# Kernel tuning notes

Measured on AMD Instinct MI355X. Metric: run time of the kernel, lower is better.

The kernel has to match this reference:

```python
import jax, jax.numpy as jnp
import numpy as np

DIM = 1024
K = 7
DILATION = 2
BATCH = 16384
NEG_SLOPE = 0.01


def setup_inputs() -> dict:
    key = jax.random.key(0)
    k1, k2, k3, k4 = jax.random.split(key, 4)
    x = jax.random.normal(k1, (BATCH, DIM), dtype=jnp.float32)
    # Conv1d(1,1,K) default init ~ U(-1/sqrt(K), 1/sqrt(K)); normal is fine for a baseline
    weight = jax.random.normal(k2, (1, 1, K), dtype=jnp.float32) * 0.3
    bias = jax.random.normal(k3, (1,), dtype=jnp.float32) * 0.1
    lmbd = jax.random.normal(k4, (DIM,), dtype=jnp.float32)
    return {"x": x, "weight": weight, "bias": bias, "lmbd": lmbd}


def _forward(x, weight, bias, lmbd):
    pad = (K - 1) * DILATION
    padded = jnp.pad(x, ((0, 0), (0, pad)))  # right-pad last dim
    # (B,1,L) conv with dilated kernel (1,1,K), VALID -> output length = DIM
    conv = jax.lax.conv_general_dilated(
        padded[:, None, :], weight,
        window_strides=(1,), padding="VALID", rhs_dilation=(DILATION,),
        dimension_numbers=("NCH", "OIH", "NCH"))
    conv = conv[:, 0, :] + bias[0]  # (B, DIM)

    w = weight.reshape(-1)  # (K,)
    w0 = w[0]

    activation = jnp.where(conv >= 0, conv, NEG_SLOPE * conv)  # leaky_relu
    act_grad = jnp.where(activation >= 0, 1.0, NEG_SLOPE)

    sp = jax.nn.softplus(lmbd)
    scale = jnp.where(w0 == 0, lmbd,
                      jnp.where(w0 > 0, -1.0 / w0 + sp, -1.0 / w0 - sp))  # (DIM,)

    # diag-matmul == broadcasted per-feature scale
    output = activation * scale + x  # skip connection
    act_grad_scaled = act_grad * scale
    logdet = jnp.log(jnp.abs(act_grad_scaled * w0 + 1.0)).sum(axis=1)  # (B,)
    return output, logdet


def reference(x, weight, bias, lmbd):
    return _forward(x, weight, bias, lmbd)
```

## Files before the change

### kernel.cpp

```cpp
#include <hip/hip_runtime.h>
#include <math.h>

#define DIM 1024
#define KK 7
#define DIL 2
#define BATCH 16384
#define NEG 0.01f
#define ROWS 8
#define RST 1040
#define NBUF 3

__device__ __forceinline__ void gload_lds16(const float* g, float* l) {
    __builtin_amdgcn_global_load_lds(
        (const __attribute__((address_space(1))) void*)g,
        (__attribute__((address_space(3))) void*)l, 16, 0, 0);
}

__global__ __launch_bounds__(256)
void cnn_flow_fused(const float* __restrict__ x,
                    const float* __restrict__ wgt,
                    const float* __restrict__ bias,
                    const float* __restrict__ lmbd,
                    float* __restrict__ out,
                    float* __restrict__ logdet) {
    const int t    = threadIdx.x;
    const int wv   = t >> 6;
    const int lane = t & 63;
    const int base = t << 2;
    const int row0 = blockIdx.x * ROWS;

    __shared__ float sx[NBUF * 2 * RST];
    __shared__ float red[ROWS][4];

    const float* gseg = x + (size_t)row0 * DIM + (wv << 8) + (lane << 2);
    float*       lseg = sx + (wv << 8) + (lane << 2);

    if (t < NBUF * 2 * 16)
        sx[(t >> 4) * RST + DIM + (t & 15)] = 0.0f;

    gload_lds16(gseg + 0 * DIM, lseg + 0 * RST);
    gload_lds16(gseg + 1 * DIM, lseg + 1 * RST);

    float w[KK];
#pragma unroll
    for (int k = 0; k < KK; ++k) w[k] = wgt[k];
    const float w0 = w[0];
    const float bs = bias[0];

    float sc[4], lp[4], ln[4];
    {
        float4 lm = *reinterpret_cast<const float4*>(lmbd + base);
        float lms[4] = {lm.x, lm.y, lm.z, lm.w};
        const float inv = (w0 != 0.0f) ? (-1.0f / w0) : 0.0f;
#pragma unroll
        for (int i = 0; i < 4; ++i) {
            float l  = lms[i];
            float sp = fmaxf(l, 0.0f) + log1pf(expf(-fabsf(l)));
            float scale;
            if (w0 == 0.0f)      scale = l;
            else if (w0 > 0.0f)  scale = inv + sp;
            else                 scale = inv - sp;
            sc[i] = scale;
            lp[i] = logf(fabsf(fmaf(scale,       w0, 1.0f)));
            ln[i] = logf(fabsf(fmaf(NEG * scale, w0, 1.0f)));
        }
    }

#pragma unroll
    for (int k = 0; k < ROWS / 2; ++k) {
        if (k < ROWS / 2 - 1) {
            float* lb = sx + ((k + 1) % NBUF) * 2 * RST + (wv << 8) + (lane << 2);
            gload_lds16(gseg + (2 * k + 2) * DIM, lb);
            gload_lds16(gseg + (2 * k + 3) * DIM, lb + RST);
        }
        if (k == 0)
            asm volatile("s_waitcnt vmcnt(2) lgkmcnt(0)" ::: "memory");
        else if (k < ROWS / 2 - 1)
            asm volatile("s_waitcnt vmcnt(4)" ::: "memory");
        else
            asm volatile("s_waitcnt vmcnt(2)" ::: "memory");
        __builtin_amdgcn_s_barrier();

        const float* buf = sx + (k % NBUF) * 2 * RST;
#pragma unroll
        for (int rr = 0; rr < 2; ++rr) {
            const int r = 2 * k + rr;
            const float* srow = buf + rr * RST + base;
            float xv[16];
#pragma unroll
            for (int j = 0; j < 4; ++j) {
                float4 v = *reinterpret_cast<const float4*>(srow + 4 * j);
                xv[4 * j + 0] = v.x; xv[4 * j + 1] = v.y;
                xv[4 * j + 2] = v.z; xv[4 * j + 3] = v.w;
            }

            float ld_acc = 0.0f;
            float o[4];
#pragma unroll
            for (int i = 0; i < 4; ++i) {
                float conv = bs;
#pragma unroll
                for (int kk = 0; kk < KK; ++kk)
                    conv = fmaf(xv[i + DIL * kk], w[kk], conv);
                bool pos  = (conv >= 0.0f);
                float act = pos ? conv : NEG * conv;
                o[i]      = fmaf(act, sc[i], xv[i]);
                ld_acc   += pos ? lp[i] : ln[i];
            }
            *reinterpret_cast<float4*>(out + (size_t)(row0 + r) * DIM + base) =
                make_float4(o[0], o[1], o[2], o[3]);

#pragma unroll
            for (int off = 32; off > 0; off >>= 1)
                ld_acc += __shfl_down(ld_acc, off, 64);
            if (lane == 0) red[r][wv] = ld_acc;
        }
    }

    __syncthreads();
    if (t < ROWS)
        logdet[row0 + t] = (red[t][0] + red[t][1]) + (red[t][2] + red[t][3]);
}

extern "C" void kernel_launch(void* const* d_in, const int* in_sizes, int n_in,
                              void* d_out, int out_size, void* d_ws, size_t ws_size,
                              hipStream_t stream) {
    const float* x    = (const float*)d_in[0];
    const float* wgt  = (const float*)d_in[1];
    const float* bias = (const float*)d_in[2];
    const float* lmbd = (const float*)d_in[3];
    float* out    = (float*)d_out;
    float* logdet = out + (size_t)BATCH * DIM;

    cnn_flow_fused<<<BATCH / ROWS, 256, 0, stream>>>(x, wgt, bias, lmbd, out, logdet);
}
```

Measured before the change: 26.83 us.

## Give each wave private LDS slots with halo loads to drop block barriers

```diff
diff --git a/kernel.cpp b/kernel.cpp
--- a/kernel.cpp
+++ b/kernel.cpp
@@ -7,13 +7,19 @@
 #define BATCH 16384
 #define NEG 0.01f
 #define ROWS 8
-#define RST 1040
 #define NBUF 3
+#define DEPTH 2
+#define SLOT 320
 
 __device__ __forceinline__ void gload_lds16(const float* g, float* l) {
     __builtin_amdgcn_global_load_lds(
         (const __attribute__((address_space(1))) void*)g,
         (__attribute__((address_space(3))) void*)l, 16, 0, 0);
+}
+__device__ __forceinline__ void gload_lds4(const float* g, float* l) {
+    __builtin_amdgcn_global_load_lds(
+        (const __attribute__((address_space(1))) void*)g,
+        (__attribute__((address_space(3))) void*)l, 4, 0, 0);
 }
 
 __global__ __launch_bounds__(256)
@@ -29,17 +35,28 @@
     const int base = t << 2;
     const int row0 = blockIdx.x * ROWS;
 
-    __shared__ float sx[NBUF * 2 * RST];
+    __shared__ float sx[4 * NBUF * SLOT];
     __shared__ float red[ROWS][4];
+    __shared__ float dummy[64];
 
-    const float* gseg = x + (size_t)row0 * DIM + (wv << 8) + (lane << 2);
-    float*       lseg = sx + (wv << 8) + (lane << 2);
+    if (wv == 3) {
+#pragma unroll
+        for (int s = 0; s < NBUF; ++s)
+            sx[(3 * NBUF + s) * SLOT + 256 + lane] = 0.0f;
+    }
 
-    if (t < NBUF * 2 * 16)
-        sx[(t >> 4) * RST + DIM + (t & 15)] = 0.0f;
+    const float* growbase = x + (size_t)row0 * DIM;
+    const float* gmain = growbase + (wv << 8) + (lane << 2);
+    const float* ghalo = growbase + ((wv < 3) ? (wv << 8) + 256 : 0) + lane;
 
-    gload_lds16(gseg + 0 * DIM, lseg + 0 * RST);
-    gload_lds16(gseg + 1 * DIM, lseg + 1 * RST);
+    auto issue_row = [&](int r) {
+        float* slot = sx + (wv * NBUF + (r % NBUF)) * SLOT;
+        gload_lds16(gmain + r * DIM, slot + (lane << 2));
+        gload_lds4(ghalo + r * DIM, ((wv < 3) ? slot + 256 : dummy) + lane);
+    };
+
+    issue_row(0);
+    issue_row(1);
 
     float w[KK];
 #pragma unroll
@@ -67,54 +84,44 @@
     }
 
 #pragma unroll
-    for (int k = 0; k < ROWS / 2; ++k) {
-        if (k < ROWS / 2 - 1) {
-            float* lb = sx + ((k + 1) % NBUF) * 2 * RST + (wv << 8) + (lane << 2);
-            gload_lds16(gseg + (2 * k + 2) * DIM, lb);
-            gload_lds16(gseg + (2 * k + 3) * DIM, lb + RST);
+    for (int r = 0; r < ROWS; ++r) {
+        if (r + DEPTH < ROWS) issue_row(r + DEPTH);
+
+        if      (r == 0) asm volatile("s_waitcnt vmcnt(4)" ::: "memory");
+        else if (r == 1) asm volatile("s_waitcnt vmcnt(5)" ::: "memory");
+        else if (r == 6) asm volatile("s_waitcnt vmcnt(4)" ::: "memory");
+        else if (r == 7) asm volatile("s_waitcnt vmcnt(2)" ::: "memory");
+        else             asm volatile("s_waitcnt vmcnt(6)" ::: "memory");
+
+        const float* srow = sx + (wv * NBUF + (r % NBUF)) * SLOT + (lane << 2);
+        float xv[16];
+#pragma unroll
+        for (int j = 0; j < 4; ++j) {
+            float4 v = *reinterpret_cast<const float4*>(srow + 4 * j);
+            xv[4 * j + 0] = v.x; xv[4 * j + 1] = v.y;
+            xv[4 * j + 2] = v.z; xv[4 * j + 3] = v.w;
         }
-        if (k == 0)
-            asm volatile("s_waitcnt vmcnt(2) lgkmcnt(0)" ::: "memory");
-        else if (k < ROWS / 2 - 1)
-            asm volatile("s_waitcnt vmcnt(4)" ::: "memory");
-        else
-            asm volatile("s_waitcnt vmcnt(2)" ::: "memory");
-        __builtin_amdgcn_s_barrier();
 
-        const float* buf = sx + (k % NBUF) * 2 * RST;
+        float ld_acc = 0.0f;
+        float o[4];
 #pragma unroll
-        for (int rr = 0; rr < 2; ++rr) {
-            const int r = 2 * k + rr;
-            const float* srow = buf + rr * RST + base;
-            float xv[16];
+        for (int i = 0; i < 4; ++i) {
+            float conv = bs;
 #pragma unroll
-            for (int j = 0; j < 4; ++j) {
-                float4 v = *reinterpret_cast<const float4*>(srow + 4 * j);
-                xv[4 * j + 0] = v.x; xv[4 * j + 1] = v.y;
-                xv[4 * j + 2] = v.z; xv[4 * j + 3] = v.w;
-            }
-
-            float ld_acc = 0.0f;
-            float o[4];
-#pragma unroll
-            for (int i = 0; i < 4; ++i) {
-                float conv = bs;
-#pragma unroll
-                for (int kk = 0; kk < KK; ++kk)
-                    conv = fmaf(xv[i + DIL * kk], w[kk], conv);
-                bool pos  = (conv >= 0.0f);
-                float act = pos ? conv : NEG * conv;
-                o[i]      = fmaf(act, sc[i], xv[i]);
-                ld_acc   += pos ? lp[i] : ln[i];
-            }
-            *reinterpret_cast<float4*>(out + (size_t)(row0 + r) * DIM + base) =
-                make_float4(o[0], o[1], o[2], o[3]);
+            for (int kk = 0; kk < KK; ++kk)
+                conv = fmaf(xv[i + DIL * kk], w[kk], conv);
+            bool pos  = (conv >= 0.0f);
+            float act = pos ? conv : NEG * conv;
+            o[i]      = fmaf(act, sc[i], xv[i]);
+            ld_acc   += pos ? lp[i] : ln[i];
+        }
+        *reinterpret_cast<float4*>(out + (size_t)(row0 + r) * DIM + base) =
+            make_float4(o[0], o[1], o[2], o[3]);
 
 #pragma unroll
-            for (int off = 32; off > 0; off >>= 1)
-                ld_acc += __shfl_down(ld_acc, off, 64);
-            if (lane == 0) red[r][wv] = ld_acc;
-        }
+        for (int off = 32; off > 0; off >>= 1)
+            ld_acc += __shfl_down(ld_acc, off, 64);
+        if (lane == 0) red[r][wv] = ld_acc;
     }
 
     __syncthreads();
```

Result: faster. 26.18 us (-2.4%).
